# Kernel tuning notes

Hardware: AMD Instinct MI355X
Metric: run time of the kernel (lower is better)

The kernel has to match this reference:

```python
import jax, jax.numpy as jnp
import numpy as np

N_HEAD = 16

def setup_inputs() -> dict:
    key = jax.random.key(0)
    ks = jax.random.split(key, 9)
    B, T, C = 1, 4096, 1024
    s = 1.0 / np.sqrt(C)
    x = jax.random.normal(ks[0], (B, T, C), dtype=jnp.float32)
    Wq = jax.random.uniform(ks[1], (C, C), jnp.float32, -s, s)
    bq = jax.random.uniform(ks[2], (C,), jnp.float32, -s, s)
    Wk = jax.random.uniform(ks[3], (C, C), jnp.float32, -s, s)
    bk = jax.random.uniform(ks[4], (C,), jnp.float32, -s, s)
    Wv = jax.random.uniform(ks[5], (C, C), jnp.float32, -s, s)
    bv = jax.random.uniform(ks[6], (C,), jnp.float32, -s, s)
    Wp = jax.random.uniform(ks[7], (C, C), jnp.float32, -s, s)
    bp = jax.random.uniform(ks[8], (C,), jnp.float32, -s, s)
    return {"x": x, "Wq": Wq, "bq": bq, "Wk": Wk, "bk": bk,
            "Wv": Wv, "bv": bv, "Wp": Wp, "bp": bp}

def reference(x, Wq, bq, Wk, bk, Wv, bv, Wp, bp):
    B, T, C = x.shape
    H = N_HEAD
    D = C // H
    # projections -> (B, H, T, D)
    def proj(W, b):
        return (x @ W.T + b).reshape(B, T, H, D).transpose(0, 2, 1, 3)
    q, k, v = proj(Wq, bq), proj(Wk, bk), proj(Wv, bv)
    scale = 1.0 / np.sqrt(D).astype(np.float32)
    att = jnp.einsum('bhtd,bhsd->bhts', q, k) * scale  # (B,H,T,T)
    causal = jnp.tril(jnp.ones((T, T), dtype=bool))
    att = jnp.where(causal[None, None], att, -jnp.inf)
    att = jax.nn.softmax(att, axis=-1)
    y = jnp.einsum('bhts,bhsd->bhtd', att, v)  # (B,H,T,D)
    y = y.transpose(0, 2, 1, 3).reshape(B, T, C)
    return y @ Wp.T + bp
```

## Files before the change

### kernel.cpp

```cpp
#include <hip/hip_runtime.h>
#include <hip/hip_bf16.h>
#include <math.h>

typedef __bf16 bf16x8 __attribute__((ext_vector_type(8)));
typedef __bf16 bf16x4 __attribute__((ext_vector_type(4)));
typedef float f32x4 __attribute__((ext_vector_type(4)));

#define MFMA_BF16 __builtin_amdgcn_mfma_f32_16x16x32_bf16

#define QSCALE 0.18033688011112042f

__device__ inline void async_load16(const __hip_bfloat16* g, __hip_bfloat16* l) {
    __builtin_amdgcn_global_load_lds(
        (const __attribute__((address_space(1))) unsigned int*)g,
        (__attribute__((address_space(3))) unsigned int*)l,
        16, 0, 0);
}

__device__ inline int sig(int x) {
    return (x & ~12) | ((x & 4) << 1) | ((x & 8) >> 1);
}

__device__ inline unsigned int pack_bf16_trunc(float lo, float hi) {
    return __builtin_amdgcn_perm(__float_as_uint(hi), __float_as_uint(lo),
                                 0x07060302u);
}

__global__ __launch_bounds__(256) void convert_all(
    const float* __restrict__ x,
    const float* __restrict__ Wq, const float* __restrict__ Wk,
    const float* __restrict__ Wv, const float* __restrict__ Wp,
    __hip_bfloat16* __restrict__ xb,
    __hip_bfloat16* __restrict__ Wqb, __hip_bfloat16* __restrict__ Wkb,
    __hip_bfloat16* __restrict__ Wvb, __hip_bfloat16* __restrict__ Wpb,
    int nx, int nw)
{
    const int xblocks = nx >> 11;
    const int wblocks = nw >> 11;
    int b = blockIdx.x;
    const float* in;
    __hip_bfloat16* out;
    int i;
    if (b < xblocks) {
        in = x; out = xb; i = (b * 256 + threadIdx.x) * 8;
    } else {
        b -= xblocks;
        const int w = b / wblocks, bb = b - w * wblocks;
        in  = w == 0 ? Wq : w == 1 ? Wk : w == 2 ? Wv : Wp;
        out = w == 0 ? Wqb : w == 1 ? Wkb : w == 2 ? Wvb : Wpb;
        i = (bb * 256 + threadIdx.x) * 8;
    }
    const float4 a = *(const float4*)(in + i);
    const float4 c = *(const float4*)(in + i + 4);
    __hip_bfloat16 tmp[8];
    tmp[0] = __float2bfloat16(a.x); tmp[1] = __float2bfloat16(a.y);
    tmp[2] = __float2bfloat16(a.z); tmp[3] = __float2bfloat16(a.w);
    tmp[4] = __float2bfloat16(c.x); tmp[5] = __float2bfloat16(c.y);
    tmp[6] = __float2bfloat16(c.z); tmp[7] = __float2bfloat16(c.w);
    *(bf16x8*)(out + i) = *(const bf16x8*)tmp;
}

__global__ __launch_bounds__(512) void gemm_qkv(
    const __hip_bfloat16* __restrict__ A,
    const __hip_bfloat16* __restrict__ B,
    const float* __restrict__ bq, const float* __restrict__ bk, const float* __restrict__ bv,
    __hip_bfloat16* __restrict__ Qo, __hip_bfloat16* __restrict__ Ko,
    __hip_bfloat16* __restrict__ Vt,
    int M, int K)
{
    __shared__ __align__(16) __hip_bfloat16 smem[2][2 * 128 * 64];

    const int tid  = threadIdx.x;
    const int lane = tid & 63;
    const int wave = tid >> 6;
    const int l15  = lane & 15;
    const int quad = lane >> 4;
    const int m0 = blockIdx.x * 128;
    const int n0 = blockIdx.y * 128;
    const int wr = wave >> 1;
    const int wc = wave & 1;
    const int sel = n0 >> 10;

    f32x4 acc[2][4] = {};

    int srow[2], scol[2];
    #pragma unroll
    for (int i = 0; i < 2; ++i) {
        const int c = tid + 512 * i;
        srow[i] = c >> 3;
        scol[i] = ((c & 7) ^ (srow[i] & 7)) * 8;
    }

    auto stageg = [&](int k0, int buf) {
        __hip_bfloat16* As = smem[buf];
        __hip_bfloat16* Bs = smem[buf] + 128 * 64;
        #pragma unroll
        for (int i = 0; i < 2; ++i) {
            async_load16(A + (size_t)(m0 + srow[i]) * K + k0 + scol[i],
                         As + (size_t)(tid + 512 * i) * 8);
            async_load16(B + (size_t)(n0 + srow[i]) * K + k0 + scol[i],
                         Bs + (size_t)(tid + 512 * i) * 8);
        }
    };

    const int NK = K >> 6;
    stageg(0, 0);

    for (int kt = 0; kt < NK; ++kt) {
        asm volatile("s_waitcnt vmcnt(0)\n\ts_barrier" ::: "memory");
        if (kt + 1 < NK) stageg((kt + 1) * 64, (kt + 1) & 1);

        const __hip_bfloat16* As = smem[kt & 1];
        const __hip_bfloat16* Bs = smem[kt & 1] + 128 * 64;

        #pragma unroll
        for (int kd = 0; kd < 2; ++kd) {
            bf16x8 af[2], bfr[4];
            #pragma unroll
            for (int mi = 0; mi < 2; ++mi) {
                const int row = wr * 32 + mi * 16 + l15;
                af[mi] = *(const bf16x8*)(
                    As + row * 64 + (((kd * 4 + quad) ^ (row & 7)) << 3));
            }
            #pragma unroll
            for (int ni = 0; ni < 4; ++ni) {
                const int row = wc * 64 + ni * 16 + l15;
                bfr[ni] = *(const bf16x8*)(
                    Bs + row * 64 + (((kd * 4 + quad) ^ (row & 7)) << 3));
            }
            #pragma unroll
            for (int mi = 0; mi < 2; ++mi)
                #pragma unroll
                for (int ni = 0; ni < 4; ++ni)
                    acc[mi][ni] = MFMA_BF16(af[mi], bfr[ni], acc[mi][ni], 0, 0, 0);
        }
    }

    if (sel == 2) {
        __hip_bfloat16* tsm = smem[0];
        __syncthreads();
        #pragma unroll
        for (int ni = 0; ni < 4; ++ni) {
            const int lc = wc * 64 + ni * 16 + l15;
            const float bias = bv[(n0 + lc) & 1023];
            #pragma unroll
            for (int mi = 0; mi < 2; ++mi) {
                const int mb = wr * 32 + mi * 16 + quad * 4;
                const int g = mb >> 3, off = mb & 7;
                __hip_bfloat16 t[4];
                #pragma unroll
                for (int r = 0; r < 4; ++r)
                    t[r] = __float2bfloat16(acc[mi][ni][r] + bias);
                *(bf16x4*)(tsm + lc * 128 + ((g ^ (lc & 15)) << 3) + off)
                    = *(const bf16x4*)t;
            }
        }
        __syncthreads();
        const int cc0 = n0 & 1023;
        #pragma unroll
        for (int i = 0; i < 4; ++i) {
            const int q = tid + 512 * i;
            const int ch = q >> 4, mg = q & 15;
            bf16x8 v = *(const bf16x8*)(tsm + ch * 128 + ((mg ^ (ch & 15)) << 3));
            *(bf16x8*)(Vt + (size_t)(cc0 + ch) * M + m0 + mg * 8) = v;
        }
    } else {
        __hip_bfloat16* dst = sel == 0 ? Qo : Ko;
        const float* bptr   = sel == 0 ? bq : bk;
        const float sc      = sel == 0 ? QSCALE : 1.0f;
        #pragma unroll
        for (int ni = 0; ni < 4; ++ni) {
            const int cc = (n0 + wc * 64 + ni * 16 + l15) & 1023;
            const float bias = bptr[cc];
            #pragma unroll
            for (int mi = 0; mi < 2; ++mi) {
                const int row = m0 + wr * 32 + mi * 16 + quad * 4;
                #pragma unroll
                for (int r = 0; r < 4; ++r)
                    dst[(size_t)(row + r) * 1024 + cc] =
                        __float2bfloat16((acc[mi][ni][r] + bias) * sc);
            }
        }
    }
}

__global__ __launch_bounds__(256) void gemm_out_f32(
    const __hip_bfloat16* __restrict__ A,
    const __hip_bfloat16* __restrict__ B,
    const float* __restrict__ bias,
    float* __restrict__ Cf,
    int M, int N, int K)
{
    __shared__ __align__(16) __hip_bfloat16 smem[2][(64 + 128) * 64];

    const int tid  = threadIdx.x;
    const int lane = tid & 63;
    const int wave = tid >> 6;
    const int l15  = lane & 15;
    const int quad = lane >> 4;
    const int m0 = blockIdx.x * 64;
    const int n0 = blockIdx.y * 128;
    const int wr = wave >> 1, wc = wave & 1;

    f32x4 acc[2][4] = {};

    int srow[4], scol[4];
    #pragma unroll
    for (int i = 0; i < 4; ++i) {
        const int c = tid + 256 * i;
        srow[i] = c >> 3;
        scol[i] = ((c & 7) ^ (srow[i] & 7)) * 8;
    }

    auto stageg = [&](int k0, int buf) {
        __hip_bfloat16* As = smem[buf];
        __hip_bfloat16* Bs = smem[buf] + 64 * 64;
        #pragma unroll
        for (int i = 0; i < 2; ++i)
            async_load16(A + (size_t)(m0 + srow[i]) * K + k0 + scol[i],
                         As + (size_t)(tid + 256 * i) * 8);
        #pragma unroll
        for (int i = 0; i < 4; ++i)
            async_load16(B + (size_t)(n0 + srow[i]) * K + k0 + scol[i],
                         Bs + (size_t)(tid + 256 * i) * 8);
    };

    const int NK = K >> 6;
    stageg(0, 0);

    for (int kt = 0; kt < NK; ++kt) {
        asm volatile("s_waitcnt vmcnt(0)\n\ts_barrier" ::: "memory");
        if (kt + 1 < NK) stageg((kt + 1) * 64, (kt + 1) & 1);

        const __hip_bfloat16* As = smem[kt & 1];
        const __hip_bfloat16* Bs = smem[kt & 1] + 64 * 64;

        #pragma unroll
        for (int kd = 0; kd < 2; ++kd) {
            bf16x8 af[2], bfr[4];
            #pragma unroll
            for (int mi = 0; mi < 2; ++mi) {
                const int row = wr * 32 + mi * 16 + l15;
                af[mi] = *(const bf16x8*)(
                    As + row * 64 + (((kd * 4 + quad) ^ (row & 7)) << 3));
            }
            #pragma unroll
            for (int ni = 0; ni < 4; ++ni) {
                const int row = wc * 64 + ni * 16 + l15;
                bfr[ni] = *(const bf16x8*)(
                    Bs + row * 64 + (((kd * 4 + quad) ^ (row & 7)) << 3));
            }
            #pragma unroll
            for (int mi = 0; mi < 2; ++mi)
                #pragma unroll
                for (int ni = 0; ni < 4; ++ni)
                    acc[mi][ni] = MFMA_BF16(af[mi], bfr[ni], acc[mi][ni], 0, 0, 0);
        }
    }

    #pragma unroll
    for (int ni = 0; ni < 4; ++ni) {
        const int col = n0 + wc * 64 + ni * 16 + l15;
        const float bv = bias[col];
        #pragma unroll
        for (int mi = 0; mi < 2; ++mi) {
            const int row = m0 + wr * 32 + mi * 16 + quad * 4;
            #pragma unroll
            for (int r = 0; r < 4; ++r)
                Cf[(size_t)(row + r) * N + col] = acc[mi][ni][r] + bv;
        }
    }
}

__global__ __launch_bounds__(512, 4) void attn_causal(
    const __hip_bfloat16* __restrict__ Q,
    const __hip_bfloat16* __restrict__ K,
    const __hip_bfloat16* __restrict__ Vt,
    __hip_bfloat16* __restrict__ PoB,
    float* __restrict__ PlB,
    int T, int C)
{
    const int nwg  = (int)(gridDim.x * gridDim.y);
    const int chunk = nwg >> 3;
    const int lin  = (int)(blockIdx.x + gridDim.x * blockIdx.y);
    const int work = (lin & 7) * chunk + (lin >> 3);
    const int h  = work >> 5;
    const int bx = work & 31;
    const int j  = bx & 7;
    const int sq = bx >> 3;
    const int tid  = threadIdx.x;
    const int w    = tid >> 6;
    const int lane = tid & 63;
    const int l15  = lane & 15;
    const int quad = lane >> 4;

    const size_t TCs = (size_t)T * C;
    const size_t HT  = (size_t)T * 16;
    __hip_bfloat16* Po = PoB + (size_t)sq * TCs;
    float* Pl = PlB + (size_t)sq * HT;

    const int len1 = j + 1, len2 = 16 - j;
    const int tile1 = j,    tile2 = 15 - j;
    const int kb1 = len1 * sq, kb2 = len2 * sq;

    __shared__ __align__(16) __hip_bfloat16 Ks[4][64 * 64];
    __shared__ __align__(16) __hip_bfloat16 Vts[4][64 * 64];

    const int r0 = tid >> 3, g0 = ((tid & 7) ^ (r0 & 7)) * 8;
    const __hip_bfloat16* Kg0 = K + (size_t)sig(r0) * C + h * 64 + g0;
    const __hip_bfloat16* Vg0 = Vt + (size_t)(h * 64 + r0) * T + g0;

    int koff[2][4], voff[2][4];
    #pragma unroll
    for (int kd = 0; kd < 2; ++kd)
        #pragma unroll
        for (int sb = 0; sb < 4; ++sb) {
            const int kappa = 32 * (sb & 1) + 8 * (l15 >> 2) + 4 * (sb >> 1) + (l15 & 3);
            const int rho = sig(kappa);
            koff[kd][sb] = rho * 64 + (((kd * 4 + quad) ^ (rho & 7)) << 3);
        }
    #pragma unroll
    for (int kk = 0; kk < 2; ++kk)
        #pragma unroll
        for (int db = 0; db < 4; ++db) {
            const int vrow = db * 16 + l15;
            voff[kk][db] = vrow * 64 + (((kk * 4 + quad) ^ (vrow & 7)) << 3);
        }

    bf16x8 ones;
    #pragma unroll
    for (int jj = 0; jj < 8; ++jj) ones[jj] = (__bf16)1.0f;

    int qbase = tile1 * 256 + w * 32;
    bf16x8 aq[2][2];
    #pragma unroll
    for (int rb = 0; rb < 2; ++rb)
        #pragma unroll
        for (int kd = 0; kd < 2; ++kd)
            aq[rb][kd] = *(const bf16x8*)(
                Q + (size_t)(qbase + rb * 16 + l15) * C + h * 64 + kd * 32 + quad * 8);

    f32x4 o[2][4] = {};
    f32x4 lacc[2] = {};

    auto stage = [&](int idx) {
        const int kb = (idx < len1) ? (kb1 + idx) : (kb2 + idx - len1);
        const size_t so = (size_t)kb << 6;
        const int sl = idx & 3;
        async_load16(Kg0 + so * C, &Ks[sl][tid * 8]);
        async_load16(Vg0 + so, &Vts[sl][tid * 8]);
    };

    stage(0);
    stage(1);

    for (int it = 0; it < 17; ++it) {
        if (it + 2 < 17) stage(it + 2);
        if (it < 15)
            asm volatile("s_waitcnt vmcnt(4)\n\ts_barrier" ::: "memory");
        else if (it == 15)
            asm volatile("s_waitcnt vmcnt(2)\n\ts_barrier" ::: "memory");
        else
            asm volatile("s_waitcnt vmcnt(0)\n\ts_barrier" ::: "memory");

        const int cur = it & 3;
        const int kb = (it < len1) ? (kb1 + it) : (kb2 + it - len1);
        const int s0 = kb << 6;

        if (it == len1) {
            #pragma unroll
            for (int rb = 0; rb < 2; ++rb) {
                const int row = qbase + rb * 16 + l15;
                #pragma unroll
                for (int db = 0; db < 4; ++db) {
                    __hip_bfloat16 t[4];
                    #pragma unroll
                    for (int r = 0; r < 4; ++r)
                        t[r] = __float2bfloat16(o[rb][db][r]);
                    *(bf16x4*)(Po + (size_t)row * C + h * 64 + db * 16 + quad * 4)
                        = *(const bf16x4*)t;
                    o[rb][db] = (f32x4){0.f, 0.f, 0.f, 0.f};
                }
                if (quad == 0)
                    Pl[(size_t)h * T + row] = lacc[rb][0];
                lacc[rb] = (f32x4){0.f, 0.f, 0.f, 0.f};
            }
            qbase = tile2 * 256 + w * 32;
            #pragma unroll
            for (int rb = 0; rb < 2; ++rb)
                #pragma unroll
                for (int kd = 0; kd < 2; ++kd)
                    aq[rb][kd] = *(const bf16x8*)(
                        Q + (size_t)(qbase + rb * 16 + l15) * C + h * 64 + kd * 32 + quad * 8);
        }

        if (s0 <= qbase + 31) {
            f32x4 sv[2][4] = {};
            #pragma unroll
            for (int kd = 0; kd < 2; ++kd)
                #pragma unroll
                for (int sb = 0; sb < 4; ++sb) {
                    bf16x8 ak = *(const bf16x8*)(&Ks[cur][koff[kd][sb]]);
                    sv[0][sb] = MFMA_BF16(ak, aq[0][kd], sv[0][sb], 0, 0, 0);
                    sv[1][sb] = MFMA_BF16(ak, aq[1][kd], sv[1][sb], 0, 0, 0);
                }

            const bool diag = (s0 + 63 > qbase);
            bf16x8 bp[2][2];
            #pragma unroll
            for (int rb = 0; rb < 2; ++rb) {
                float pv[4][4];
                #pragma unroll
                for (int sb = 0; sb < 4; ++sb)
                    #pragma unroll
                    for (int r = 0; r < 4; ++r)
                        pv[sb][r] = __builtin_amdgcn_exp2f(sv[rb][sb][r]);
                if (diag) {
                    const int thr = qbase + rb * 16 + l15 - s0 - 8 * quad;
                    #pragma unroll
                    for (int sb = 0; sb < 4; ++sb)
                        #pragma unroll
                        for (int r = 0; r < 4; ++r) {
                            const int c = 32 * (sb & 1) + 4 * (sb >> 1) + r;
                            pv[sb][r] = (c <= thr) ? pv[sb][r] : 0.f;
                        }
                }
                #pragma unroll
                for (int kk = 0; kk < 2; ++kk) {
                    union { unsigned int u[4]; bf16x8 v; } pk;
                    pk.u[0] = pack_bf16_trunc(pv[kk][0], pv[kk][1]);
                    pk.u[1] = pack_bf16_trunc(pv[kk][2], pv[kk][3]);
                    pk.u[2] = pack_bf16_trunc(pv[kk + 2][0], pv[kk + 2][1]);
                    pk.u[3] = pack_bf16_trunc(pv[kk + 2][2], pv[kk + 2][3]);
                    bp[rb][kk] = pk.v;
                }
            }

            lacc[0] = MFMA_BF16(ones, bp[0][0], lacc[0], 0, 0, 0);
            lacc[0] = MFMA_BF16(ones, bp[0][1], lacc[0], 0, 0, 0);
            lacc[1] = MFMA_BF16(ones, bp[1][0], lacc[1], 0, 0, 0);
            lacc[1] = MFMA_BF16(ones, bp[1][1], lacc[1], 0, 0, 0);

            #pragma unroll
            for (int kk = 0; kk < 2; ++kk)
                #pragma unroll
                for (int db = 0; db < 4; ++db) {
                    bf16x8 av = *(const bf16x8*)(&Vts[cur][voff[kk][db]]);
                    o[0][db] = MFMA_BF16(av, bp[0][kk], o[0][db], 0, 0, 0);
                    o[1][db] = MFMA_BF16(av, bp[1][kk], o[1][db], 0, 0, 0);
                }
        }
    }

    #pragma unroll
    for (int rb = 0; rb < 2; ++rb) {
        const int row = qbase + rb * 16 + l15;
        #pragma unroll
        for (int db = 0; db < 4; ++db) {
            __hip_bfloat16 t[4];
            #pragma unroll
            for (int r = 0; r < 4; ++r)
                t[r] = __float2bfloat16(o[rb][db][r]);
            *(bf16x4*)(Po + (size_t)row * C + h * 64 + db * 16 + quad * 4)
                = *(const bf16x4*)t;
        }
        if (quad == 0)
            Pl[(size_t)h * T + row] = lacc[rb][0];
    }
}

__global__ __launch_bounds__(256) void merge_y(
    const __hip_bfloat16* __restrict__ PoB, const float* __restrict__ PlB,
    __hip_bfloat16* __restrict__ Y, int T, int C)
{
    const size_t i = ((size_t)blockIdx.x * 256 + threadIdx.x) * 8;
    const int row = (int)(i / C);
    const int h   = ((int)(i % C)) >> 6;
    const size_t TC = (size_t)T * C;
    const size_t HT = (size_t)T * 16;
    float acc[8] = {};
    float l = 0.f;
    #pragma unroll
    for (int z = 0; z < 4; ++z) {
        bf16x8 a = *(const bf16x8*)(PoB + z * TC + i);
        #pragma unroll
        for (int r = 0; r < 8; ++r)
            acc[r] += (float)(((const __bf16*)&a)[r]);
        l += PlB[z * HT + (size_t)h * T + row];
    }
    const float inv = 1.0f / l;
    __hip_bfloat16 t[8];
    #pragma unroll
    for (int r = 0; r < 8; ++r)
        t[r] = __float2bfloat16(acc[r] * inv);
    *(bf16x8*)(Y + i) = *(const bf16x8*)t;
}

extern "C" void kernel_launch(void* const* d_in, const int* in_sizes, int n_in,
                              void* d_out, int out_size, void* d_ws, size_t ws_size,
                              hipStream_t stream)
{
    const float* x  = (const float*)d_in[0];
    const float* Wq = (const float*)d_in[1];
    const float* bq = (const float*)d_in[2];
    const float* Wk = (const float*)d_in[3];
    const float* bk = (const float*)d_in[4];
    const float* Wv = (const float*)d_in[5];
    const float* bv = (const float*)d_in[6];
    const float* Wp = (const float*)d_in[7];
    const float* bp = (const float*)d_in[8];

    const int C = 1024;
    const int T = in_sizes[0] / C;
    const int H = 16;
    const size_t TC = (size_t)T * C;
    const size_t CC = (size_t)C * C;

    __hip_bfloat16* xb  = (__hip_bfloat16*)d_ws;
    __hip_bfloat16* Wqb = xb + TC;
    __hip_bfloat16* Wkb = Wqb + CC;
    __hip_bfloat16* Wvb = Wkb + CC;
    __hip_bfloat16* Wpb = Wvb + CC;
    __hip_bfloat16* Qw  = Wpb + CC;
    __hip_bfloat16* Kw  = Qw + TC;
    __hip_bfloat16* Vtw = Kw + TC;
    __hip_bfloat16* PoB = Vtw + TC;
    float* PlB = (float*)(PoB + 4 * TC);
    __hip_bfloat16* Yw  = xb;
    float* out = (float*)d_out;

    convert_all<<<(int)(TC / 2048 + 4 * CC / 2048), 256, 0, stream>>>(
        x, Wq, Wk, Wv, Wp, xb, Wqb, Wkb, Wvb, Wpb, (int)TC, (int)CC);

    gemm_qkv<<<dim3(T / 128, 3072 / 128), 512, 0, stream>>>(
        xb, Wqb, bq, bk, bv, Qw, Kw, Vtw, T, C);

    attn_causal<<<dim3(32, H), 512, 0, stream>>>(
        Qw, Kw, Vtw, PoB, PlB, T, C);

    merge_y<<<(int)(TC / 8 / 256), 256, 0, stream>>>(
        PoB, PlB, Yw, T, C);

    gemm_out_f32<<<dim3(T / 64, C / 128), 256, 0, stream>>>(
        Yw, Wpb, bp, out, T, C, C);
}
```

Measured before the change: 185.2 us.

## Enlarge attention query tile to 64 rows per wave, halving grid

Each wave now handles 64 query rows (4 row blocks) instead of 32, so a workgroup covers 512 query rows and each K/V tile loaded into LDS is reused across twice as many queries. The grid shrinks from 32x16 to 16x16 workgroups, and the paired-tile causal schedule is remapped to 8 tiles with 18 iterations. The intent is to cut K/V global/LDS traffic per unit of work. In exchange, register pressure rises (occupancy hint lowered from 4 to 2), and the smaller grid of 256 workgroups may leave compute units underfilled.

```diff
diff --git a/kernel.cpp b/kernel.cpp
--- a/kernel.cpp
+++ b/kernel.cpp
@@ -272,7 +272,7 @@
     }
 }
 
-__global__ __launch_bounds__(512, 4) void attn_causal(
+__global__ __launch_bounds__(512, 2) void attn_causal(
     const __hip_bfloat16* __restrict__ Q,
     const __hip_bfloat16* __restrict__ K,
     const __hip_bfloat16* __restrict__ Vt,
@@ -284,10 +284,10 @@
     const int chunk = nwg >> 3;
     const int lin  = (int)(blockIdx.x + gridDim.x * blockIdx.y);
     const int work = (lin & 7) * chunk + (lin >> 3);
-    const int h  = work >> 5;
-    const int bx = work & 31;
-    const int j  = bx & 7;
-    const int sq = bx >> 3;
+    const int h  = work >> 4;
+    const int bx = work & 15;
+    const int j  = bx & 3;
+    const int sq = bx >> 2;
     const int tid  = threadIdx.x;
     const int w    = tid >> 6;
     const int lane = tid & 63;
@@ -299,9 +299,9 @@
     __hip_bfloat16* Po = PoB + (size_t)sq * TCs;
     float* Pl = PlB + (size_t)sq * HT;
 
-    const int len1 = j + 1, len2 = 16 - j;
-    const int tile1 = j,    tile2 = 15 - j;
-    const int kb1 = len1 * sq, kb2 = len2 * sq;
+    const int len1 = 2 * (j + 1), len2 = 2 * (8 - j);
+    const int tile1 = j,           tile2 = 7 - j;
+    const int kb1 = len1 * sq,     kb2 = len2 * sq;
 
     __shared__ __align__(16) __hip_bfloat16 Ks[4][64 * 64];
     __shared__ __align__(16) __hip_bfloat16 Vts[4][64 * 64];
@@ -330,18 +330,7 @@
     bf16x8 ones;
     #pragma unroll
     for (int jj = 0; jj < 8; ++jj) ones[jj] = (__bf16)1.0f;
-
-    int qbase = tile1 * 256 + w * 32;
-    bf16x8 aq[2][2];
-    #pragma unroll
-    for (int rb = 0; rb < 2; ++rb)
-        #pragma unroll
-        for (int kd = 0; kd < 2; ++kd)
-            aq[rb][kd] = *(const bf16x8*)(
-                Q + (size_t)(qbase + rb * 16 + l15) * C + h * 64 + kd * 32 + quad * 8);
-
-    f32x4 o[2][4] = {};
-    f32x4 lacc[2] = {};
+    const f32x4 z4 = {0.f, 0.f, 0.f, 0.f};
 
     auto stage = [&](int idx) {
         const int kb = (idx < len1) ? (kb1 + idx) : (kb2 + idx - len1);
@@ -354,11 +343,23 @@
     stage(0);
     stage(1);
 
-    for (int it = 0; it < 17; ++it) {
-        if (it + 2 < 17) stage(it + 2);
-        if (it < 15)
+    int qbase = tile1 * 512 + w * 64;
+    bf16x8 aq[4][2];
+    #pragma unroll
+    for (int rb = 0; rb < 4; ++rb)
+        #pragma unroll
+        for (int kd = 0; kd < 2; ++kd)
+            aq[rb][kd] = *(const bf16x8*)(
+                Q + (size_t)(qbase + rb * 16 + l15) * C + h * 64 + kd * 32 + quad * 8);
+
+    f32x4 o[4][4] = {};
+    f32x4 lacc[4] = {};
+
+    for (int it = 0; it < 18; ++it) {
+        if (it + 2 < 18) stage(it + 2);
+        if (it < 16)
             asm volatile("s_waitcnt vmcnt(4)\n\ts_barrier" ::: "memory");
-        else if (it == 15)
+        else if (it == 16)
             asm volatile("s_waitcnt vmcnt(2)\n\ts_barrier" ::: "memory");
         else
             asm volatile("s_waitcnt vmcnt(0)\n\ts_barrier" ::: "memory");
@@ -369,7 +370,7 @@
 
         if (it == len1) {
             #pragma unroll
-            for (int rb = 0; rb < 2; ++rb) {
+            for (int rb = 0; rb < 4; ++rb) {
                 const int row = qbase + rb * 16 + l15;
                 #pragma unroll
                 for (int db = 0; db < 4; ++db) {
@@ -385,36 +386,39 @@
                     Pl[(size_t)h * T + row] = lacc[rb][0];
                 lacc[rb] = (f32x4){0.f, 0.f, 0.f, 0.f};
             }
-            qbase = tile2 * 256 + w * 32;
-            #pragma unroll
-            for (int rb = 0; rb < 2; ++rb)
+            qbase = tile2 * 512 + w * 64;
+            #pragma unroll
+            for (int rb = 0; rb < 4; ++rb)
                 #pragma unroll
                 for (int kd = 0; kd < 2; ++kd)
                     aq[rb][kd] = *(const bf16x8*)(
                         Q + (size_t)(qbase + rb * 16 + l15) * C + h * 64 + kd * 32 + quad * 8);
         }
 
-        if (s0 <= qbase + 31) {
-            f32x4 sv[2][4] = {};
+        if (s0 <= qbase + 63) {
+            bf16x8 ak[2][4];
             #pragma unroll
             for (int kd = 0; kd < 2; ++kd)
                 #pragma unroll
-                for (int sb = 0; sb < 4; ++sb) {
-                    bf16x8 ak = *(const bf16x8*)(&Ks[cur][koff[kd][sb]]);
-                    sv[0][sb] = MFMA_BF16(ak, aq[0][kd], sv[0][sb], 0, 0, 0);
-                    sv[1][sb] = MFMA_BF16(ak, aq[1][kd], sv[1][sb], 0, 0, 0);
-                }
+                for (int sb = 0; sb < 4; ++sb)
+                    ak[kd][sb] = *(const bf16x8*)(&Ks[cur][koff[kd][sb]]);
 
             const bool diag = (s0 + 63 > qbase);
-            bf16x8 bp[2][2];
-            #pragma unroll
-            for (int rb = 0; rb < 2; ++rb) {
+            bf16x8 bp[4][2];
+            #pragma unroll
+            for (int rb = 0; rb < 4; ++rb) {
+                f32x4 sv[4];
+                #pragma unroll
+                for (int sb = 0; sb < 4; ++sb)
+                    sv[sb] = MFMA_BF16(ak[1][sb], aq[rb][1],
+                                 MFMA_BF16(ak[0][sb], aq[rb][0], z4, 0, 0, 0),
+                                 0, 0, 0);
                 float pv[4][4];
                 #pragma unroll
                 for (int sb = 0; sb < 4; ++sb)
                     #pragma unroll
                     for (int r = 0; r < 4; ++r)
-                        pv[sb][r] = __builtin_amdgcn_exp2f(sv[rb][sb][r]);
+                        pv[sb][r] = __builtin_amdgcn_exp2f(sv[sb][r]);
                 if (diag) {
                     const int thr = qbase + rb * 16 + l15 - s0 - 8 * quad;
                     #pragma unroll
@@ -436,24 +440,26 @@
                 }
             }
 
-            lacc[0] = MFMA_BF16(ones, bp[0][0], lacc[0], 0, 0, 0);
-            lacc[0] = MFMA_BF16(ones, bp[0][1], lacc[0], 0, 0, 0);
-            lacc[1] = MFMA_BF16(ones, bp[1][0], lacc[1], 0, 0, 0);
-            lacc[1] = MFMA_BF16(ones, bp[1][1], lacc[1], 0, 0, 0);
+            #pragma unroll
+            for (int rb = 0; rb < 4; ++rb) {
+                lacc[rb] = MFMA_BF16(ones, bp[rb][0], lacc[rb], 0, 0, 0);
+                lacc[rb] = MFMA_BF16(ones, bp[rb][1], lacc[rb], 0, 0, 0);
+            }
 
             #pragma unroll
             for (int kk = 0; kk < 2; ++kk)
                 #pragma unroll
                 for (int db = 0; db < 4; ++db) {
                     bf16x8 av = *(const bf16x8*)(&Vts[cur][voff[kk][db]]);
-                    o[0][db] = MFMA_BF16(av, bp[0][kk], o[0][db], 0, 0, 0);
-                    o[1][db] = MFMA_BF16(av, bp[1][kk], o[1][db], 0, 0, 0);
+                    #pragma unroll
+                    for (int rb = 0; rb < 4; ++rb)
+                        o[rb][db] = MFMA_BF16(av, bp[rb][kk], o[rb][db], 0, 0, 0);
                 }
         }
     }
 
     #pragma unroll
-    for (int rb = 0; rb < 2; ++rb) {
+    for (int rb = 0; rb < 4; ++rb) {
         const int row = qbase + rb * 16 + l15;
         #pragma unroll
         for (int db = 0; db < 4; ++db) {
@@ -535,7 +541,7 @@
     gemm_qkv<<<dim3(T / 128, 3072 / 128), 512, 0, stream>>>(
         xb, Wqb, bq, bk, bv, Qw, Kw, Vtw, T, C);
 
-    attn_causal<<<dim3(32, H), 512, 0, stream>>>(
+    attn_causal<<<dim3(16, H), 512, 0, stream>>>(
         Qw, Kw, Vtw, PoB, PlB, T, C);
 
     merge_y<<<(int)(TC / 8 / 256), 256, 0, stream>>>(
```

After: 186.9 us. Within noise of the previous version (+0.9%).
